# Optimization experiments

Measured on AMD Instinct MI355X. Metric: run time of the kernel, lower is better.

The kernel has to match this reference:

```python
import jax, jax.numpy as jnp
import numpy as np

DIM = 256
QK_DIM = 256
NUM_HEADS = 8
N_WIN = 7
TOPK = 4
SCALE = QK_DIM ** (-0.5)


def setup_inputs() -> dict:
    key = jax.random.key(0)
    k1, k2, k3 = jax.random.split(key, 3)
    N, D, H, W, C = 2, 8, 56, 56, DIM
    x = jax.random.normal(k1, (N, D, H, W, C), dtype=jnp.float32)
    # QKVLinear: Linear(dim, qk_dim + qk_dim + dim)
    Wqkv = jax.random.normal(k2, (C, 2 * QK_DIM + DIM), dtype=jnp.float32) * 0.02
    bqkv = jnp.zeros((2 * QK_DIM + DIM,), dtype=jnp.float32)
    Wo = jax.random.normal(k3, (DIM, DIM), dtype=jnp.float32) * 0.02
    bo = jnp.zeros((DIM,), dtype=jnp.float32)
    return {"x": x, "Wqkv": Wqkv, "bqkv": bqkv, "Wo": Wo, "bo": bo}


def reference(x, Wqkv, bqkv, Wo, bo):
    N, D, H, W, C = x.shape
    j = i = N_WIN
    h, w = H // j, W // i
    p2, w2 = j * i, h * w
    n = N * D
    m = NUM_HEADS
    ch = QK_DIM // m   # qk head dim
    cv = DIM // m      # v head dim

    # n t (j h) (i w) c -> n t (j i) h w c
    xw = x.reshape(N, D, j, h, i, w, C).transpose(0, 1, 2, 4, 3, 5, 6)
    xw = xw.reshape(N, D, p2, h, w, C)

    # QKVLinear then split into q / kv
    qkv = xw @ Wqkv + bqkv                       # (N,D,p2,h,w,2qk+dim)
    q = qkv[..., :QK_DIM]                        # (N,D,p2,h,w,qk)
    kv = qkv[..., QK_DIM:]                       # (N,D,p2,h,w,qk+dim)

    # inter-frame shift: frame t uses kv of frame t+1; last frame keeps its own
    kv = jnp.concatenate([kv[:, 1:], kv[:, -1:]], axis=1)

    q = q.reshape(n, p2, h, w, QK_DIM)
    kv = kv.reshape(n, p2, h, w, QK_DIM + DIM)
    q_pix = q.reshape(n, p2, w2, QK_DIM)
    kv_pix = kv.reshape(n, p2, w2, QK_DIM + DIM)  # identity kv_down

    # window-level routing (diff_routing=False -> detached)
    q_win = jax.lax.stop_gradient(q.mean(axis=(2, 3)))                  # (n,p2,qk)
    k_win = jax.lax.stop_gradient(kv[..., :QK_DIM].mean(axis=(2, 3)))   # (n,p2,qk)
    attn_logit = jnp.einsum('npc,nqc->npq', q_win * SCALE, k_win)       # (n,p2,p2)
    topk_logit, r_idx = jax.lax.top_k(attn_logit, TOPK)                 # (n,p2,topk)
    r_weight = jax.nn.softmax(topk_logit, axis=-1)  # computed, unused (mul_weight='none')

    # gather kv of routed windows: (n,p2,topk,w2,qk+dim)
    kv_sel = jax.vmap(lambda kvp, idx: kvp[idx])(kv_pix, r_idx)

    k_sel = kv_sel[..., :QK_DIM].reshape(n, p2, TOPK * w2, m, ch)
    v_sel = kv_sel[..., QK_DIM:].reshape(n, p2, TOPK * w2, m, cv)
    qh = q_pix.reshape(n, p2, w2, m, ch)

    attn = jnp.einsum('npqmc,npkmc->npmqk', qh * SCALE, k_sel)  # (n,p2,m,w2,topk*w2)
    attn = jax.nn.softmax(attn, axis=-1)
    out = jnp.einsum('npmqk,npkmc->npqmc', attn, v_sel).reshape(n, p2, w2, C)

    # (n j i) (h w) c -> N D (j h) (i w) c
    out = out.reshape(N, D, j, i, h, w, C).transpose(0, 1, 2, 4, 3, 5, 6)
    out = out.reshape(N, D, H, W, C)
    out = out @ Wo + bo
    return out
```

## Files before the change

kernel.cpp:

```cpp
#include <hip/hip_runtime.h>
#include <hip/hip_bf16.h>
#include <math.h>

#define QSC 0.09016844f

typedef __attribute__((ext_vector_type(8))) short bf16x8;
typedef __attribute__((ext_vector_type(4))) float f32x4;

__device__ __forceinline__ ushort f2bf(float f) {
    unsigned u = __float_as_uint(f);
    return (ushort)((u + 0x7FFFu + ((u >> 16) & 1u)) >> 16);
}

__device__ __forceinline__ unsigned pk2bf(float a, float b) {
    __hip_bfloat162 h = __float22bfloat162_rn(make_float2(a, b));
    return *(unsigned*)&h;
}

__device__ __forceinline__ void gl_lds16(const ushort* g, ushort* l) {
    __builtin_amdgcn_global_load_lds(
        (const __attribute__((address_space(1))) unsigned int*)g,
        (__attribute__((address_space(3))) unsigned int*)l, 16, 0, 0);
}

__device__ __forceinline__ int swz(int row) { return (row ^ (row >> 2)) & 3; }

__global__ __launch_bounds__(256) void k_prep(const float* __restrict__ x,
                                              const float* __restrict__ Wqkv,
                                              const float* __restrict__ Wo,
                                              ushort* __restrict__ xg,
                                              float* __restrict__ xmean,
                                              ushort* __restrict__ Wqkvt,
                                              ushort* __restrict__ Wot) {
    int b = blockIdx.x;
    int tid = threadIdx.x;
    if (b >= 784) {
        int bb = b - 784;
        if (bb < 768) Wqkvt[bb * 256 + tid] = f2bf(Wqkv[(size_t)tid * 768 + bb]);
        else { int n = bb - 768; Wot[n * 256 + tid] = f2bf(Wo[(size_t)tid * 256 + n]); }
        return;
    }
    int nd = b / 49, p = b % 49;
    int j = p / 7, i = p % 7;
    const float* xb = x + ((size_t)nd * 3136 + (j * 8) * 56 + i * 8) * 256 + tid;
    ushort* xo = xg + (size_t)b * 64 * 256 + tid;
    float s = 0.f;
#pragma unroll 2
    for (int hh = 0; hh < 8; ++hh)
#pragma unroll
        for (int ww = 0; ww < 8; ++ww) {
            float v = xb[(size_t)(hh * 56 + ww) * 256];
            s += v;
            xo[(size_t)(hh * 8 + ww) * 256] = f2bf(v);
        }
    xmean[(size_t)b * 256 + tid] = s * (1.f / 64.f);
}

__global__ __launch_bounds__(256) void k_winproj(const float* __restrict__ xmean,
                                                 const float* __restrict__ Wqkv,
                                                 const float* __restrict__ bqkv,
                                                 float* __restrict__ qwin,
                                                 float* __restrict__ kwin) {
    __shared__ float As[16 * 68];
    __shared__ float Bs[16 * 64];
    const int tid = threadIdx.x;
    const int m0 = blockIdx.y * 64;
    const int n0 = blockIdx.x * 64;

    const int ar = tid >> 2;
    const int ak = (tid & 3) * 4;
    const int arow = (m0 + ar < 784) ? (m0 + ar) : 783;
    const float* aptr = xmean + (size_t)arow * 256 + ak;

    const int bk = tid >> 4;
    const int bn = (tid & 15) * 4;
    const float* bptr = Wqkv + (size_t)bk * 768 + n0 + bn;

    const int ty = tid >> 4, tx = tid & 15;
    float acc[4][4] = {};

    for (int kt = 0; kt < 256; kt += 16) {
        float4 av = *(const float4*)(aptr + kt);
        float4 bv = *(const float4*)(bptr + (size_t)kt * 768);
        __syncthreads();
        As[(ak + 0) * 68 + ar] = av.x;
        As[(ak + 1) * 68 + ar] = av.y;
        As[(ak + 2) * 68 + ar] = av.z;
        As[(ak + 3) * 68 + ar] = av.w;
        *(float4*)&Bs[bk * 64 + bn] = bv;
        __syncthreads();
#pragma unroll
        for (int kk = 0; kk < 16; ++kk) {
            float4 a4 = *(const float4*)&As[kk * 68 + ty * 4];
            float4 b4 = *(const float4*)&Bs[kk * 64 + tx * 4];
            float a[4] = {a4.x, a4.y, a4.z, a4.w};
            float b[4] = {b4.x, b4.y, b4.z, b4.w};
#pragma unroll
            for (int ii = 0; ii < 4; ++ii)
#pragma unroll
                for (int jj = 0; jj < 4; ++jj) acc[ii][jj] += a[ii] * b[jj];
        }
    }
#pragma unroll
    for (int ii = 0; ii < 4; ++ii) {
        int t = m0 + ty * 4 + ii;
        if (t >= 784) continue;
#pragma unroll
        for (int jj = 0; jj < 4; ++jj) {
            int col = n0 + tx * 4 + jj;
            float v = acc[ii][jj] + bqkv[col];
            if (col < 256) qwin[(size_t)t * 256 + col] = v;
            else           kwin[(size_t)t * 256 + (col - 256)] = v;
        }
    }
}

__global__ __launch_bounds__(256) void k_route(const float* __restrict__ qwin,
                                               const float* __restrict__ kwin,
                                               int* __restrict__ ridx) {
    const int b = blockIdx.x;
    const int nd = b / 49;
    const int ndkv = ((nd & 7) == 7) ? nd : nd + 1;
    const int tid = threadIdx.x;
    const int t = tid & 63, w = tid >> 6;
    __shared__ float qs[256];
    __shared__ float part[4][64];
    qs[tid] = qwin[b * 256 + tid];
    __syncthreads();
    float s = 0.f;
    if (t < 49) {
        const float* kr = kwin + ((size_t)ndkv * 49 + t) * 256 + w * 64;
#pragma unroll
        for (int c = 0; c < 64; c += 4) {
            float4 k4 = *(const float4*)(kr + c);
            float4 q4 = *(const float4*)&qs[w * 64 + c];
            s += q4.x * k4.x + q4.y * k4.y + q4.z * k4.z + q4.w * k4.w;
        }
    }
    part[w][t] = s;
    __syncthreads();
    if (tid < 64) {
        float logit = (t < 49) ? (part[0][t] + part[1][t] + part[2][t] + part[3][t])
                               : -INFINITY;
        for (int sel = 0; sel < 4; ++sel) {
            float v = logit;
            int ix = t;
            for (int off = 32; off > 0; off >>= 1) {
                float ov = __shfl_xor(v, off);
                int   oi = __shfl_xor(ix, off);
                if (ov > v || (ov == v && oi < ix)) { v = ov; ix = oi; }
            }
            if (t == 0) ridx[b * 4 + sel] = ix;
            if (t == ix) logit = -INFINITY;
        }
    }
}

__global__ __launch_bounds__(256) void k_gemm_qkv(const ushort* __restrict__ A,
                                                  const ushort* __restrict__ Bt,
                                                  const float* __restrict__ bqkv,
                                                  ushort* __restrict__ q,
                                                  ushort* __restrict__ kv) {
    __shared__ ushort As[2][128 * 32];
    __shared__ ushort Bs[2][128 * 32];
    const int tid = threadIdx.x;
    const int wv = tid >> 6, ln = tid & 63;
    const int lane15 = ln & 15, quad = ln >> 4;

    const int lin  = blockIdx.x + blockIdx.y * 6;
    const int work = (lin & 7) * 294 + (lin >> 3);
    const int n0 = (work % 6) * 128;
    const int m0 = (work / 6) * 128;

    const int row0 = tid >> 2, ck0 = tid & 3;
    const ushort* gA[2]; const ushort* gB[2];
    int lofs[2];
#pragma unroll
    for (int p = 0; p < 2; ++p) {
        int r = p * 64 + row0;
        int cks = ck0 ^ swz(r);
        gA[p] = A  + (size_t)(m0 + r) * 256 + cks * 8;
        gB[p] = Bt + (size_t)(n0 + r) * 256 + cks * 8;
        lofs[p] = (p * 256 + tid) * 8;
    }

    f32x4 acc[4][4];
#pragma unroll
    for (int i = 0; i < 4; ++i)
#pragma unroll
        for (int j = 0; j < 4; ++j) acc[i][j] = (f32x4){0.f, 0.f, 0.f, 0.f};

    const int mb = (wv >> 1) * 64, nb = (wv & 1) * 64;

#pragma unroll
    for (int p = 0; p < 2; ++p) {
        gl_lds16(gA[p], &As[0][lofs[p]]);
        gl_lds16(gB[p], &Bs[0][lofs[p]]);
    }
    asm volatile("s_waitcnt vmcnt(0)" ::: "memory");
    __builtin_amdgcn_s_barrier();

    int cur = 0;
#pragma unroll
    for (int kt = 0; kt < 8; ++kt) {
        if (kt < 7) {
#pragma unroll
            for (int p = 0; p < 2; ++p) {
                gl_lds16(gA[p] + (kt + 1) * 32, &As[cur ^ 1][lofs[p]]);
                gl_lds16(gB[p] + (kt + 1) * 32, &Bs[cur ^ 1][lofs[p]]);
            }
        }
        __builtin_amdgcn_sched_barrier(0);
        bf16x8 aF[4], bF[4];
#pragma unroll
        for (int mt = 0; mt < 4; ++mt) {
            int r = mb + mt * 16 + lane15;
            aF[mt] = *(const bf16x8*)&As[cur][r * 32 + (quad ^ swz(r)) * 8];
        }
#pragma unroll
        for (int nt = 0; nt < 4; ++nt) {
            int r = nb + nt * 16 + lane15;
            bF[nt] = *(const bf16x8*)&Bs[cur][r * 32 + (quad ^ swz(r)) * 8];
        }
#pragma unroll
        for (int mt = 0; mt < 4; ++mt)
#pragma unroll
            for (int nt = 0; nt < 4; ++nt)
                acc[mt][nt] = __builtin_amdgcn_mfma_f32_16x16x32_bf16(aF[mt], bF[nt], acc[mt][nt], 0, 0, 0);
        __builtin_amdgcn_sched_barrier(0);
        asm volatile("s_waitcnt vmcnt(0)" ::: "memory");
        __builtin_amdgcn_s_barrier();
        cur ^= 1;
    }

#pragma unroll
    for (int mt = 0; mt < 4; ++mt) {
#pragma unroll
        for (int nt = 0; nt < 4; ++nt) {
            int col = n0 + nb + nt * 16 + lane15;
            float bias = bqkv[col];
#pragma unroll
            for (int r = 0; r < 4; ++r) {
                int t = m0 + mb + mt * 16 + quad * 4 + r;
                float v = acc[mt][nt][r] + bias;
                if (col < 256) q[(size_t)t * 256 + col] = f2bf(v * QSC);
                else           kv[(size_t)t * 512 + (col - 256)] = f2bf(v);
            }
        }
    }
}

__global__ __launch_bounds__(256) void k_gemm_o(const ushort* __restrict__ A,
                                                const ushort* __restrict__ Bt,
                                                const float* __restrict__ bo,
                                                float* __restrict__ out) {
    __shared__ ushort As[2][128 * 32];
    __shared__ ushort Bs[2][128 * 32];
    const int tid = threadIdx.x;
    const int wv = tid >> 6, ln = tid & 63;
    const int lane15 = ln & 15, quad = ln >> 4;

    const int lin  = blockIdx.x;
    const int work = (lin & 7) * 98 + (lin >> 3);
    const int n0 = (work % 2) * 128;
    const int m0 = (work / 2) * 128;

    const int row0 = tid >> 2, ck0 = tid & 3;
    const ushort* gA[2]; const ushort* gB[2];
    int lofs[2];
#pragma unroll
    for (int p = 0; p < 2; ++p) {
        int r = p * 64 + row0;
        int cks = ck0 ^ swz(r);
        gA[p] = A  + (size_t)(m0 + r) * 256 + cks * 8;
        gB[p] = Bt + (size_t)(n0 + r) * 256 + cks * 8;
        lofs[p] = (p * 256 + tid) * 8;
    }

    f32x4 acc[4][4];
#pragma unroll
    for (int i = 0; i < 4; ++i)
#pragma unroll
        for (int j = 0; j < 4; ++j) acc[i][j] = (f32x4){0.f, 0.f, 0.f, 0.f};

    const int mb = (wv >> 1) * 64, nb = (wv & 1) * 64;

#pragma unroll
    for (int p = 0; p < 2; ++p) {
        gl_lds16(gA[p], &As[0][lofs[p]]);
        gl_lds16(gB[p], &Bs[0][lofs[p]]);
    }
    asm volatile("s_waitcnt vmcnt(0)" ::: "memory");
    __builtin_amdgcn_s_barrier();

    int cur = 0;
#pragma unroll
    for (int kt = 0; kt < 8; ++kt) {
        if (kt < 7) {
#pragma unroll
            for (int p = 0; p < 2; ++p) {
                gl_lds16(gA[p] + (kt + 1) * 32, &As[cur ^ 1][lofs[p]]);
                gl_lds16(gB[p] + (kt + 1) * 32, &Bs[cur ^ 1][lofs[p]]);
            }
        }
        __builtin_amdgcn_sched_barrier(0);
        bf16x8 aF[4], bF[4];
#pragma unroll
        for (int mt = 0; mt < 4; ++mt) {
            int r = mb + mt * 16 + lane15;
            aF[mt] = *(const bf16x8*)&As[cur][r * 32 + (quad ^ swz(r)) * 8];
        }
#pragma unroll
        for (int nt = 0; nt < 4; ++nt) {
            int r = nb + nt * 16 + lane15;
            bF[nt] = *(const bf16x8*)&Bs[cur][r * 32 + (quad ^ swz(r)) * 8];
        }
#pragma unroll
        for (int mt = 0; mt < 4; ++mt)
#pragma unroll
            for (int nt = 0; nt < 4; ++nt)
                acc[mt][nt] = __builtin_amdgcn_mfma_f32_16x16x32_bf16(aF[mt], bF[nt], acc[mt][nt], 0, 0, 0);
        __builtin_amdgcn_sched_barrier(0);
        asm volatile("s_waitcnt vmcnt(0)" ::: "memory");
        __builtin_amdgcn_s_barrier();
        cur ^= 1;
    }

    const int w6 = (m0 + mb) >> 6;
    const int ndw = w6 / 49, pw = w6 % 49;
    const int wbase = ndw * 3136 + (pw / 7) * 8 * 56 + (pw % 7) * 8;
#pragma unroll
    for (int mt = 0; mt < 4; ++mt)
#pragma unroll
        for (int nt = 0; nt < 4; ++nt) {
            int col = n0 + nb + nt * 16 + lane15;
            float bias = bo[col];
#pragma unroll
            for (int r = 0; r < 4; ++r) {
                int pix = mt * 16 + quad * 4 + r;
                int xr = wbase + (pix >> 3) * 56 + (pix & 7);
                out[(size_t)xr * 256 + col] = acc[mt][nt][r] + bias;
            }
        }
}

__global__ __launch_bounds__(256, 3) void k_attn(ushort* qbuf,
                                                 const ushort* __restrict__ kvbuf,
                                                 const int* __restrict__ ridx) {
    const int lin  = blockIdx.x + (blockIdx.y + blockIdx.z * 49) * 8;
    const int work = (lin & 7) * 784 + (lin >> 3);
    const int h = work & 7;
    const int rest = work >> 3;
    const int p = rest % 49;
    const int nd = rest / 49;

    const int ndkv = ((nd & 7) == 7) ? nd : nd + 1;
    const int tid = threadIdx.x;
    const int wv = tid >> 6, ln = tid & 63;
    const int lane15 = ln & 15, quad = ln >> 4;

    __shared__ ushort Ks[256 * 32];
    __shared__ ushort Vt[32 * 264];
    __shared__ ushort Ps[64 * 72];

    const int rb = (nd * 49 + p) * 4;
    int wid[4];
#pragma unroll
    for (int i = 0; i < 4; ++i) wid[i] = ridx[rb + i];

    const size_t kvband = (size_t)ndkv * 49;

    {
        const int key_l = wv * 16 + (ln >> 2);
        const int ck = (ln ^ (ln >> 2) ^ (ln >> 4)) & 3;
#pragma unroll
        for (int i = 0; i < 4; ++i) {
            size_t trow = (kvband + wid[i]) * 64 + key_l;
            gl_lds16(kvbuf + trow * 512 + h * 32 + ck * 8,
                     &Ks[(i * 64 + wv * 16) * 32 + ln * 8]);
        }
    }

    const size_t qrow0 = (size_t)(nd * 49 + p) * 64;
    bf16x8 bQ = *(const bf16x8*)(qbuf + (qrow0 + wv * 16 + lane15) * 256 + h * 32 + quad * 8);

    {
        int key_l = (tid & 31) * 2;
        int ch0 = (tid >> 5) * 4;
#pragma unroll
        for (int i = 0; i < 4; ++i) {
            size_t trow = (kvband + wid[i]) * 64;
            const ushort* g0 = kvbuf + (trow + key_l) * 512 + 256 + h * 32 + ch0;
            const ushort* g1 = g0 + 512;
            ushort4 a = *(const ushort4*)g0;
            ushort4 b = *(const ushort4*)g1;
            int kg = i * 64 + key_l;
            *(unsigned*)&Vt[(ch0 + 0) * 264 + kg] = (unsigned)a.x | ((unsigned)b.x << 16);
            *(unsigned*)&Vt[(ch0 + 1) * 264 + kg] = (unsigned)a.y | ((unsigned)b.y << 16);
            *(unsigned*)&Vt[(ch0 + 2) * 264 + kg] = (unsigned)a.z | ((unsigned)b.z << 16);
            *(unsigned*)&Vt[(ch0 + 3) * 264 + kg] = (unsigned)a.w | ((unsigned)b.w << 16);
        }
    }

    __syncthreads();

    const int ksz = (lane15 ^ (lane15 >> 2)) & 3;
    f32x4 st[16];
    __builtin_amdgcn_s_setprio(1);
#pragma unroll
    for (int t = 0; t < 16; ++t) {
        bf16x8 aK = *(const bf16x8*)&Ks[(t * 16 + lane15) * 32 + (quad ^ ksz) * 8];
        st[t] = __builtin_amdgcn_mfma_f32_16x16x32_bf16(aK, bQ, (f32x4){0.f, 0.f, 0.f, 0.f}, 0, 0, 0);
    }
    __builtin_amdgcn_s_setprio(0);

    float sum = 0.f;
#pragma unroll
    for (int t = 0; t < 16; ++t)
#pragma unroll
        for (int r = 0; r < 4; ++r) {
            float e = __builtin_amdgcn_exp2f(st[t][r]);
            st[t][r] = e;
            sum += e;
        }
    sum += __shfl_xor(sum, 16);
    sum += __shfl_xor(sum, 32);
    const float inv = 1.f / sum;

    f32x4 oacc[2] = {{0.f, 0.f, 0.f, 0.f}, {0.f, 0.f, 0.f, 0.f}};
    const int prow = (wv * 16 + lane15) * 72;
#pragma unroll
    for (int cc = 0; cc < 4; ++cc) {
#pragma unroll
        for (int tt = 0; tt < 4; ++tt) {
            int t = cc * 4 + tt;
            uint2 pk;
            pk.x = pk2bf(st[t][0], st[t][1]);
            pk.y = pk2bf(st[t][2], st[t][3]);
            *(uint2*)&Ps[prow + tt * 16 + quad * 4] = pk;
        }
        __builtin_amdgcn_s_setprio(1);
#pragma unroll
        for (int kt = 0; kt < 2; ++kt) {
            bf16x8 aP = *(const bf16x8*)&Ps[prow + kt * 32 + quad * 8];
#pragma unroll
            for (int nt = 0; nt < 2; ++nt) {
                bf16x8 bV = *(const bf16x8*)&Vt[(nt * 16 + lane15) * 264 + cc * 64 + kt * 32 + quad * 8];
                oacc[nt] = __builtin_amdgcn_mfma_f32_16x16x32_bf16(aP, bV, oacc[nt], 0, 0, 0);
            }
        }
        __builtin_amdgcn_s_setprio(0);
    }

#pragma unroll
    for (int nt = 0; nt < 2; ++nt)
#pragma unroll
        for (int r = 0; r < 4; ++r) {
            int row = wv * 16 + quad * 4 + r;
            qbuf[(qrow0 + row) * 256 + h * 32 + nt * 16 + lane15] = f2bf(oacc[nt][r] * inv);
        }
}

extern "C" void kernel_launch(void* const* d_in, const int* in_sizes, int n_in,
                              void* d_out, int out_size, void* d_ws, size_t ws_size,
                              hipStream_t stream) {
    const float* x    = (const float*)d_in[0];
    const float* Wqkv = (const float*)d_in[1];
    const float* bqkv = (const float*)d_in[2];
    const float* Wo   = (const float*)d_in[3];
    const float* bo   = (const float*)d_in[4];
    float* out = (float*)d_out;

    char* ws = (char*)d_ws;
    ushort* xg    = (ushort*)ws;                    ws += (size_t)50176 * 256 * 2;
    ushort* q     = (ushort*)ws;                    ws += (size_t)50176 * 256 * 2;
    ushort* kv    = (ushort*)ws;                    ws += (size_t)50176 * 512 * 2;
    ushort* Wqkvt = (ushort*)ws;                    ws += (size_t)768 * 256 * 2;
    ushort* Wot   = (ushort*)ws;                    ws += (size_t)256 * 256 * 2;
    float*  xmean = (float*)ws;                     ws += (size_t)784 * 256 * 4;
    float*  qwin  = (float*)ws;                     ws += (size_t)784 * 256 * 4;
    float*  kwin  = (float*)ws;                     ws += (size_t)784 * 256 * 4;
    int*    ridx  = (int*)ws;

    k_prep    <<<1808, 256, 0, stream>>>(x, Wqkv, Wo, xg, xmean, Wqkvt, Wot);
    k_winproj <<<dim3(8, 13), 256, 0, stream>>>(xmean, Wqkv, bqkv, qwin, kwin);
    k_route   <<<784, 256, 0, stream>>>(qwin, kwin, ridx);
    k_gemm_qkv<<<dim3(6, 392), 256, 0, stream>>>(xg, Wqkvt, bqkv, q, kv);
    k_attn    <<<dim3(8, 49, 16), 256, 0, stream>>>(q, kv, ridx);
    k_gemm_o  <<<784, 256, 0, stream>>>(q, Wot, bo, out);
}
```

Before: 232.9 us.

## Fuse windowed attention and output projection into one kernel per window

Merges the attention kernel and the output GEMM. Each block now handles one (frame, window) pair, loops over all 8 heads in turn, and keeps the 64x256 attention output in LDS, then multiplies it by Wo directly from global memory. This removes the round trip of the attention output through global memory and one kernel launch. In exchange there are far fewer blocks (784 vs 6272), the heads are processed one after another with barriers between them, LDS use is higher, and the Wo operand is read from global memory with no LDS tiling.

```diff
diff --git a/kernel.cpp b/kernel.cpp
--- a/kernel.cpp
+++ b/kernel.cpp
@@ -250,109 +250,16 @@
     }
 }
 
-__global__ __launch_bounds__(256) void k_gemm_o(const ushort* __restrict__ A,
-                                                const ushort* __restrict__ Bt,
+__global__ __launch_bounds__(256) void k_attn_o(const ushort* __restrict__ qbuf,
+                                                const ushort* __restrict__ kvbuf,
+                                                const int* __restrict__ ridx,
+                                                const ushort* __restrict__ Wot,
                                                 const float* __restrict__ bo,
                                                 float* __restrict__ out) {
-    __shared__ ushort As[2][128 * 32];
-    __shared__ ushort Bs[2][128 * 32];
-    const int tid = threadIdx.x;
-    const int wv = tid >> 6, ln = tid & 63;
-    const int lane15 = ln & 15, quad = ln >> 4;
-
     const int lin  = blockIdx.x;
     const int work = (lin & 7) * 98 + (lin >> 3);
-    const int n0 = (work % 2) * 128;
-    const int m0 = (work / 2) * 128;
-
-    const int row0 = tid >> 2, ck0 = tid & 3;
-    const ushort* gA[2]; const ushort* gB[2];
-    int lofs[2];
-#pragma unroll
-    for (int p = 0; p < 2; ++p) {
-        int r = p * 64 + row0;
-        int cks = ck0 ^ swz(r);
-        gA[p] = A  + (size_t)(m0 + r) * 256 + cks * 8;
-        gB[p] = Bt + (size_t)(n0 + r) * 256 + cks * 8;
-        lofs[p] = (p * 256 + tid) * 8;
-    }
-
-    f32x4 acc[4][4];
-#pragma unroll
-    for (int i = 0; i < 4; ++i)
-#pragma unroll
-        for (int j = 0; j < 4; ++j) acc[i][j] = (f32x4){0.f, 0.f, 0.f, 0.f};
-
-    const int mb = (wv >> 1) * 64, nb = (wv & 1) * 64;
-
-#pragma unroll
-    for (int p = 0; p < 2; ++p) {
-        gl_lds16(gA[p], &As[0][lofs[p]]);
-        gl_lds16(gB[p], &Bs[0][lofs[p]]);
-    }
-    asm volatile("s_waitcnt vmcnt(0)" ::: "memory");
-    __builtin_amdgcn_s_barrier();
-
-    int cur = 0;
-#pragma unroll
-    for (int kt = 0; kt < 8; ++kt) {
-        if (kt < 7) {
-#pragma unroll
-            for (int p = 0; p < 2; ++p) {
-                gl_lds16(gA[p] + (kt + 1) * 32, &As[cur ^ 1][lofs[p]]);
-                gl_lds16(gB[p] + (kt + 1) * 32, &Bs[cur ^ 1][lofs[p]]);
-            }
-        }
-        __builtin_amdgcn_sched_barrier(0);
-        bf16x8 aF[4], bF[4];
-#pragma unroll
-        for (int mt = 0; mt < 4; ++mt) {
-            int r = mb + mt * 16 + lane15;
-            aF[mt] = *(const bf16x8*)&As[cur][r * 32 + (quad ^ swz(r)) * 8];
-        }
-#pragma unroll
-        for (int nt = 0; nt < 4; ++nt) {
-            int r = nb + nt * 16 + lane15;
-            bF[nt] = *(const bf16x8*)&Bs[cur][r * 32 + (quad ^ swz(r)) * 8];
-        }
-#pragma unroll
-        for (int mt = 0; mt < 4; ++mt)
-#pragma unroll
-            for (int nt = 0; nt < 4; ++nt)
-                acc[mt][nt] = __builtin_amdgcn_mfma_f32_16x16x32_bf16(aF[mt], bF[nt], acc[mt][nt], 0, 0, 0);
-        __builtin_amdgcn_sched_barrier(0);
-        asm volatile("s_waitcnt vmcnt(0)" ::: "memory");
-        __builtin_amdgcn_s_barrier();
-        cur ^= 1;
-    }
-
-    const int w6 = (m0 + mb) >> 6;
-    const int ndw = w6 / 49, pw = w6 % 49;
-    const int wbase = ndw * 3136 + (pw / 7) * 8 * 56 + (pw % 7) * 8;
-#pragma unroll
-    for (int mt = 0; mt < 4; ++mt)
-#pragma unroll
-        for (int nt = 0; nt < 4; ++nt) {
-            int col = n0 + nb + nt * 16 + lane15;
-            float bias = bo[col];
-#pragma unroll
-            for (int r = 0; r < 4; ++r) {
-                int pix = mt * 16 + quad * 4 + r;
-                int xr = wbase + (pix >> 3) * 56 + (pix & 7);
-                out[(size_t)xr * 256 + col] = acc[mt][nt][r] + bias;
-            }
-        }
-}
-
-__global__ __launch_bounds__(256, 3) void k_attn(ushort* qbuf,
-                                                 const ushort* __restrict__ kvbuf,
-                                                 const int* __restrict__ ridx) {
-    const int lin  = blockIdx.x + (blockIdx.y + blockIdx.z * 49) * 8;
-    const int work = (lin & 7) * 784 + (lin >> 3);
-    const int h = work & 7;
-    const int rest = work >> 3;
-    const int p = rest % 49;
-    const int nd = rest / 49;
+    const int p  = work % 49;
+    const int nd = work / 49;
 
     const int ndkv = ((nd & 7) == 7) ? nd : nd + 1;
     const int tid = threadIdx.x;
@@ -362,6 +269,7 @@
     __shared__ ushort Ks[256 * 32];
     __shared__ ushort Vt[32 * 264];
     __shared__ ushort Ps[64 * 72];
+    __shared__ ushort Qp[64 * 264];
 
     const int rb = (nd * 49 + p) * 4;
     int wid[4];
@@ -369,96 +277,127 @@
     for (int i = 0; i < 4; ++i) wid[i] = ridx[rb + i];
 
     const size_t kvband = (size_t)ndkv * 49;
-
-    {
-        const int key_l = wv * 16 + (ln >> 2);
-        const int ck = (ln ^ (ln >> 2) ^ (ln >> 4)) & 3;
+    const size_t qrow0  = (size_t)(nd * 49 + p) * 64;
+
+    const int key_l = wv * 16 + (ln >> 2);
+    const int ckst  = (ln ^ (ln >> 2) ^ (ln >> 4)) & 3;
+    const int ksz   = (lane15 ^ (lane15 >> 2)) & 3;
+    const int vkey  = (tid & 31) * 2;
+    const int vch0  = (tid >> 5) * 4;
+
+    for (int h = 0; h < 8; ++h) {
+        if (h > 0) __builtin_amdgcn_s_barrier();
+
 #pragma unroll
         for (int i = 0; i < 4; ++i) {
             size_t trow = (kvband + wid[i]) * 64 + key_l;
-            gl_lds16(kvbuf + trow * 512 + h * 32 + ck * 8,
+            gl_lds16(kvbuf + trow * 512 + h * 32 + ckst * 8,
                      &Ks[(i * 64 + wv * 16) * 32 + ln * 8]);
         }
-    }
-
-    const size_t qrow0 = (size_t)(nd * 49 + p) * 64;
-    bf16x8 bQ = *(const bf16x8*)(qbuf + (qrow0 + wv * 16 + lane15) * 256 + h * 32 + quad * 8);
-
-    {
-        int key_l = (tid & 31) * 2;
-        int ch0 = (tid >> 5) * 4;
+
+        bf16x8 bQ = *(const bf16x8*)(qbuf + (qrow0 + wv * 16 + lane15) * 256 + h * 32 + quad * 8);
+
 #pragma unroll
         for (int i = 0; i < 4; ++i) {
             size_t trow = (kvband + wid[i]) * 64;
-            const ushort* g0 = kvbuf + (trow + key_l) * 512 + 256 + h * 32 + ch0;
+            const ushort* g0 = kvbuf + (trow + vkey) * 512 + 256 + h * 32 + vch0;
             const ushort* g1 = g0 + 512;
             ushort4 a = *(const ushort4*)g0;
             ushort4 b = *(const ushort4*)g1;
-            int kg = i * 64 + key_l;
-            *(unsigned*)&Vt[(ch0 + 0) * 264 + kg] = (unsigned)a.x | ((unsigned)b.x << 16);
-            *(unsigned*)&Vt[(ch0 + 1) * 264 + kg] = (unsigned)a.y | ((unsigned)b.y << 16);
-            *(unsigned*)&Vt[(ch0 + 2) * 264 + kg] = (unsigned)a.z | ((unsigned)b.z << 16);
-            *(unsigned*)&Vt[(ch0 + 3) * 264 + kg] = (unsigned)a.w | ((unsigned)b.w << 16);
-        }
-    }
-
-    __syncthreads();
-
-    const int ksz = (lane15 ^ (lane15 >> 2)) & 3;
-    f32x4 st[16];
-    __builtin_amdgcn_s_setprio(1);
-#pragma unroll
-    for (int t = 0; t < 16; ++t) {
-        bf16x8 aK = *(const bf16x8*)&Ks[(t * 16 + lane15) * 32 + (quad ^ ksz) * 8];
-        st[t] = __builtin_amdgcn_mfma_f32_16x16x32_bf16(aK, bQ, (f32x4){0.f, 0.f, 0.f, 0.f}, 0, 0, 0);
-    }
-    __builtin_amdgcn_s_setprio(0);
-
-    float sum = 0.f;
-#pragma unroll
-    for (int t = 0; t < 16; ++t)
-#pragma unroll
-        for (int r = 0; r < 4; ++r) {
-            float e = __builtin_amdgcn_exp2f(st[t][r]);
-            st[t][r] = e;
-            sum += e;
-        }
-    sum += __shfl_xor(sum, 16);
-    sum += __shfl_xor(sum, 32);
-    const float inv = 1.f / sum;
-
-    f32x4 oacc[2] = {{0.f, 0.f, 0.f, 0.f}, {0.f, 0.f, 0.f, 0.f}};
-    const int prow = (wv * 16 + lane15) * 72;
-#pragma unroll
-    for (int cc = 0; cc < 4; ++cc) {
-#pragma unroll
-        for (int tt = 0; tt < 4; ++tt) {
-            int t = cc * 4 + tt;
-            uint2 pk;
-            pk.x = pk2bf(st[t][0], st[t][1]);
-            pk.y = pk2bf(st[t][2], st[t][3]);
-            *(uint2*)&Ps[prow + tt * 16 + quad * 4] = pk;
-        }
+            int kg = i * 64 + vkey;
+            *(unsigned*)&Vt[(vch0 + 0) * 264 + kg] = (unsigned)a.x | ((unsigned)b.x << 16);
+            *(unsigned*)&Vt[(vch0 + 1) * 264 + kg] = (unsigned)a.y | ((unsigned)b.y << 16);
+            *(unsigned*)&Vt[(vch0 + 2) * 264 + kg] = (unsigned)a.z | ((unsigned)b.z << 16);
+            *(unsigned*)&Vt[(vch0 + 3) * 264 + kg] = (unsigned)a.w | ((unsigned)b.w << 16);
+        }
+
+        asm volatile("s_waitcnt vmcnt(0) lgkmcnt(0)" ::: "memory");
+        __builtin_amdgcn_s_barrier();
+
+        f32x4 st[16];
         __builtin_amdgcn_s_setprio(1);
 #pragma unroll
-        for (int kt = 0; kt < 2; ++kt) {
-            bf16x8 aP = *(const bf16x8*)&Ps[prow + kt * 32 + quad * 8];
-#pragma unroll
-            for (int nt = 0; nt < 2; ++nt) {
-                bf16x8 bV = *(const bf16x8*)&Vt[(nt * 16 + lane15) * 264 + cc * 64 + kt * 32 + quad * 8];
-                oacc[nt] = __builtin_amdgcn_mfma_f32_16x16x32_bf16(aP, bV, oacc[nt], 0, 0, 0);
-            }
+        for (int t = 0; t < 16; ++t) {
+            bf16x8 aK = *(const bf16x8*)&Ks[(t * 16 + lane15) * 32 + (quad ^ ksz) * 8];
+            st[t] = __builtin_amdgcn_mfma_f32_16x16x32_bf16(aK, bQ, (f32x4){0.f, 0.f, 0.f, 0.f}, 0, 0, 0);
         }
         __builtin_amdgcn_s_setprio(0);
-    }
-
-#pragma unroll
-    for (int nt = 0; nt < 2; ++nt)
-#pragma unroll
-        for (int r = 0; r < 4; ++r) {
-            int row = wv * 16 + quad * 4 + r;
-            qbuf[(qrow0 + row) * 256 + h * 32 + nt * 16 + lane15] = f2bf(oacc[nt][r] * inv);
-        }
+
+        float sum = 0.f;
+#pragma unroll
+        for (int t = 0; t < 16; ++t)
+#pragma unroll
+            for (int r = 0; r < 4; ++r) {
+                float e = __builtin_amdgcn_exp2f(st[t][r]);
+                st[t][r] = e;
+                sum += e;
+            }
+        sum += __shfl_xor(sum, 16);
+        sum += __shfl_xor(sum, 32);
+        const float inv = 1.f / sum;
+
+        f32x4 oacc[2] = {{0.f, 0.f, 0.f, 0.f}, {0.f, 0.f, 0.f, 0.f}};
+        const int prow = (wv * 16 + lane15) * 72;
+#pragma unroll
+        for (int cc = 0; cc < 4; ++cc) {
+#pragma unroll
+            for (int tt = 0; tt < 4; ++tt) {
+                int t = cc * 4 + tt;
+                uint2 pk;
+                pk.x = pk2bf(st[t][0], st[t][1]);
+                pk.y = pk2bf(st[t][2], st[t][3]);
+                *(uint2*)&Ps[prow + tt * 16 + quad * 4] = pk;
+            }
+            __builtin_amdgcn_s_setprio(1);
+#pragma unroll
+            for (int kt = 0; kt < 2; ++kt) {
+                bf16x8 aP = *(const bf16x8*)&Ps[prow + kt * 32 + quad * 8];
+#pragma unroll
+                for (int nt = 0; nt < 2; ++nt) {
+                    bf16x8 bV = *(const bf16x8*)&Vt[(nt * 16 + lane15) * 264 + cc * 64 + kt * 32 + quad * 8];
+                    oacc[nt] = __builtin_amdgcn_mfma_f32_16x16x32_bf16(aP, bV, oacc[nt], 0, 0, 0);
+                }
+            }
+            __builtin_amdgcn_s_setprio(0);
+        }
+
+#pragma unroll
+        for (int nt = 0; nt < 2; ++nt)
+#pragma unroll
+            for (int r = 0; r < 4; ++r) {
+                int row = wv * 16 + quad * 4 + r;
+                Qp[row * 264 + h * 32 + nt * 16 + lane15] = f2bf(oacc[nt][r] * inv);
+            }
+    }
+
+    bf16x8 aF[8];
+#pragma unroll
+    for (int kt = 0; kt < 8; ++kt)
+        aF[kt] = *(const bf16x8*)&Qp[(wv * 16 + lane15) * 264 + kt * 32 + quad * 8];
+
+    const int wbase = nd * 3136 + (p / 7) * 8 * 56 + (p % 7) * 8;
+    int xr4[4];
+#pragma unroll
+    for (int r = 0; r < 4; ++r) {
+        int pix = wv * 16 + quad * 4 + r;
+        xr4[r] = wbase + (pix >> 3) * 56 + (pix & 7);
+    }
+
+#pragma unroll
+    for (int nt = 0; nt < 16; ++nt) {
+        const ushort* bp = Wot + (size_t)(nt * 16 + lane15) * 256 + quad * 8;
+        f32x4 acc = (f32x4){0.f, 0.f, 0.f, 0.f};
+#pragma unroll
+        for (int kt = 0; kt < 8; ++kt) {
+            bf16x8 bF = *(const bf16x8*)(bp + kt * 32);
+            acc = __builtin_amdgcn_mfma_f32_16x16x32_bf16(aF[kt], bF, acc, 0, 0, 0);
+        }
+        int col = nt * 16 + lane15;
+        float bias = bo[col];
+#pragma unroll
+        for (int r = 0; r < 4; ++r)
+            out[(size_t)xr4[r] * 256 + col] = acc[r] + bias;
+    }
 }
 
 extern "C" void kernel_launch(void* const* d_in, const int* in_sizes, int n_in,
@@ -486,6 +425,5 @@
     k_winproj <<<dim3(8, 13), 256, 0, stream>>>(xmean, Wqkv, bqkv, qwin, kwin);
     k_route   <<<784, 256, 0, stream>>>(qwin, kwin, ridx);
     k_gemm_qkv<<<dim3(6, 392), 256, 0, stream>>>(xg, Wqkvt, bqkv, q, kv);
-    k_attn    <<<dim3(8, 49, 16), 256, 0, stream>>>(q, kv, ridx);
-    k_gemm_o  <<<784, 256, 0, stream>>>(q, Wot, bo, out);
-}
+    k_attn_o  <<<784, 256, 0, stream>>>(q, kv, ridx, Wot, bo, out);
+}
```

New measurement: 292.0 us. 25.4% more time.
